# Kernel tuning notes

Measured on AMD Instinct MI355X. Metric: run time of the kernel, lower is better.

## Reference

```python
import jax, jax.numpy as jnp
import numpy as np


def setup_inputs() -> dict:
    key = jax.random.key(0)
    B, n, E, D = 128, 128, 524288, 64  # graphs, nodes/graph, original edges, edge-feat dim
    k1, k2, k3, k4 = jax.random.split(key, 4)
    g = jax.random.randint(k1, (E,), 0, B)
    src = jax.random.randint(k2, (E,), 0, n)
    dst = jax.random.randint(k3, (E,), 0, n)
    edge_index = jnp.stack([g * n + src, g * n + dst]).astype(jnp.int32)  # [2,E], within-graph edges
    edge_attr = jax.random.normal(k4, (E, D), dtype=jnp.float32)
    batch = jnp.repeat(jnp.arange(B, dtype=jnp.int32), n)  # [N] node -> graph id
    return {"edge_index": edge_index, "edge_attr": edge_attr, "batch": batch,
            "num_graphs": B, "n_per_graph": n}


def reference(edge_index, edge_attr, batch, num_graphs, n_per_graph):
    """Pad edge set to the full per-graph adjacency (incl. self-loops, as the
    torch code's ones().nonzero() does) and coalesce with op='add'.
    Equal-sized graphs => full edge list has static shape [2, B*n*n], already
    unique and row-major sorted, matching torch_sparse.coalesce output order."""
    B, n = num_graphs, n_per_graph
    D = edge_attr.shape[1]
    gid = jnp.arange(B, dtype=edge_index.dtype)[:, None, None]  # [B,1,1]
    loc = jnp.arange(n, dtype=edge_index.dtype)
    rows = jnp.broadcast_to(gid * n + loc[None, :, None], (B, n, n)).reshape(-1)
    cols = jnp.broadcast_to(gid * n + loc[None, None, :], (B, n, n)).reshape(-1)
    out_idx = jnp.stack([rows, cols])  # [2, B*n*n]
    # position of each original edge inside the full (sorted) edge list
    r, c = edge_index[0], edge_index[1]
    g = batch[r].astype(r.dtype)
    pos = g * (n * n) + (r - g * n) * n + (c - g * n)  # [E]
    # coalesce op='add': zeros for padded edges, sum original attrs on duplicates
    out_val = jnp.zeros((B * n * n, D), dtype=edge_attr.dtype).at[pos].add(edge_attr)
    return out_idx, out_val
```

## Files before the change

kernel.cpp:

```cpp
#include <hip/hip_runtime.h>


typedef float vfloat4 __attribute__((ext_vector_type(4)));

__global__ void build_chain_kernel(const int* __restrict__ ei,
                                   const int* __restrict__ batch,
                                   int* __restrict__ head,
                                   int* __restrict__ next,
                                   int E, int n, int n2) {
    int e = blockIdx.x * blockDim.x + threadIdx.x;
    if (e >= E) return;
    int r = ei[e];
    int c = ei[E + e];
    int g = batch[r];
    int pos = g * n2 + (r - g * n) * n + (c - g * n);
    next[e] = atomicExch(&head[pos], e);
}

template <int CHUNKS>
__global__ void gather_occupied_kernel(const float* __restrict__ ea,
                                       const int* __restrict__ head,
                                       const int* __restrict__ next,
                                       float* __restrict__ vals,
                                       int M, int D) {
    unsigned tid = blockIdx.x * blockDim.x + threadIdx.x;
    unsigned q, ch;
    if (CHUNKS > 0) {
        q = tid / (unsigned)CHUNKS;
        ch = tid & (unsigned)(CHUNKS - 1);
    } else {
        unsigned chunks = (unsigned)(D >> 2);
        q = tid / chunks;
        ch = tid - q * chunks;
    }
    if (q >= (unsigned)M) return;

    int e = head[q];
    if (e < 0) return;

    vfloat4 acc = {0.f, 0.f, 0.f, 0.f};
    do {
        const vfloat4 v = *(const vfloat4*)(ea + (size_t)e * D + ch * 4);
        acc += v;
        e = next[e];
    } while (e >= 0);
    __builtin_nontemporal_store(acc, (vfloat4*)(vals + (size_t)q * D + ch * 4));
}

__global__ void fill_idx_kernel(float* __restrict__ rows,
                                float* __restrict__ cols,
                                int M, int n, int n2) {
    int q0 = (blockIdx.x * blockDim.x + threadIdx.x) * 4;
    if (q0 >= M) return;
    float4 rv, cv;
    int q = q0;
    rv.x = (float)(q / n); cv.x = (float)((q / n2) * n + (q % n)); q++;
    rv.y = (float)(q / n); cv.y = (float)((q / n2) * n + (q % n)); q++;
    rv.z = (float)(q / n); cv.z = (float)((q / n2) * n + (q % n)); q++;
    rv.w = (float)(q / n); cv.w = (float)((q / n2) * n + (q % n));
    *(float4*)(rows + q0) = rv;
    *(float4*)(cols + q0) = cv;
}

__global__ void scatter_add_kernel(const int* __restrict__ ei,
                                   const float* __restrict__ ea,
                                   const int* __restrict__ batch,
                                   float* __restrict__ vals,
                                   int E, int D, int n, int n2) {
    int chunksPerEdge = D >> 2;
    long long tid = (long long)blockIdx.x * blockDim.x + threadIdx.x;
    int e = (int)(tid / chunksPerEdge);
    int ch = (int)(tid % chunksPerEdge);
    if (e >= E) return;
    int r = ei[e];
    int c = ei[E + e];
    int g = batch[r];
    long long pos = (long long)g * n2 + (long long)(r - g * n) * n + (long long)(c - g * n);
    float4 src = *(const float4*)(ea + (long long)e * D + ch * 4);
    float* dst = vals + pos * D + ch * 4;
    atomicAdd(dst + 0, src.x);
    atomicAdd(dst + 1, src.y);
    atomicAdd(dst + 2, src.z);
    atomicAdd(dst + 3, src.w);
}

extern "C" void kernel_launch(void* const* d_in, const int* in_sizes, int n_in,
                              void* d_out, int out_size, void* d_ws, size_t ws_size,
                              hipStream_t stream) {
    const int* edge_index = (const int*)d_in[0];
    const float* edge_attr = (const float*)d_in[1];
    const int* batch = (const int*)d_in[2];

    const int E  = in_sizes[0] / 2;
    const int D  = in_sizes[1] / E;
    const int M  = out_size / (D + 2);
    const int BN = in_sizes[2];
    const int n  = M / BN;
    const int n2 = n * n;

    float* rows = (float*)d_out;
    float* cols = rows + M;
    float* vals = cols + M;

    const size_t ws_need = ((size_t)M + (size_t)E) * sizeof(int);
    if (ws_size >= ws_need && (D & 3) == 0) {
        int* head = (int*)d_ws;
        int* next = head + M;

        (void)hipMemsetAsync(vals, 0, (size_t)M * D * sizeof(float), stream);
        (void)hipMemsetAsync(head, 0xFF, (size_t)M * sizeof(int), stream);

        {
            int block = 256;
            int grid = (E + block - 1) / block;
            build_chain_kernel<<<grid, block, 0, stream>>>(
                edge_index, batch, head, next, E, n, n2);
        }
        {
            long long total = (long long)M * (D / 4);
            int block = 256;
            long long grid = (total + block - 1) / block;
            if (D == 64) {
                gather_occupied_kernel<16><<<(int)grid, block, 0, stream>>>(
                    edge_attr, head, next, vals, M, D);
            } else {
                gather_occupied_kernel<0><<<(int)grid, block, 0, stream>>>(
                    edge_attr, head, next, vals, M, D);
            }
        }
        {
            int threads = (M + 3) / 4;
            int block = 256;
            int grid = (threads + block - 1) / block;
            fill_idx_kernel<<<grid, block, 0, stream>>>(rows, cols, M, n, n2);
        }
    } else {
        (void)hipMemsetAsync(vals, 0, (size_t)M * D * sizeof(float), stream);
        {
            int threads = (M + 3) / 4;
            int block = 256;
            int grid = (threads + block - 1) / block;
            fill_idx_kernel<<<grid, block, 0, stream>>>(rows, cols, M, n, n2);
        }
        {
            long long total = (long long)E * (D / 4);
            int block = 256;
            long long grid = (total + block - 1) / block;
            scatter_add_kernel<<<(int)grid, block, 0, stream>>>(
                edge_index, edge_attr, batch, vals, E, D, n, n2);
        }
    }
}
```

Before: 732.0 us.

## Fuse zero-fill into gather kernel and use grid-stride loop

Removes the separate memset of the output values and has the gather kernel write zeros for empty adjacency slots itself, so each output element is written once. The gather becomes a grid-stride loop capped at 8192 blocks, with the next-pointer load issued before the accumulate. The aim is to avoid a second full pass over the large output buffer. In exchange every slot is now visited and stored by the kernel, including empty ones, and the capped grid may give less latency hiding.

```diff
diff --git a/kernel.cpp b/kernel.cpp
--- a/kernel.cpp
+++ b/kernel.cpp
@@ -18,33 +18,34 @@
 }
 
 template <int CHUNKS>
-__global__ void gather_occupied_kernel(const float* __restrict__ ea,
-                                       const int* __restrict__ head,
-                                       const int* __restrict__ next,
-                                       float* __restrict__ vals,
-                                       int M, int D) {
-    unsigned tid = blockIdx.x * blockDim.x + threadIdx.x;
-    unsigned q, ch;
-    if (CHUNKS > 0) {
-        q = tid / (unsigned)CHUNKS;
-        ch = tid & (unsigned)(CHUNKS - 1);
-    } else {
-        unsigned chunks = (unsigned)(D >> 2);
-        q = tid / chunks;
-        ch = tid - q * chunks;
+__global__ __launch_bounds__(256) void fused_vals_kernel(
+        const float* __restrict__ ea,
+        const int* __restrict__ head,
+        const int* __restrict__ next,
+        float* __restrict__ vals,
+        long long total, int D) {
+    const long long stride = (long long)gridDim.x * blockDim.x;
+    for (long long tid = (long long)blockIdx.x * blockDim.x + threadIdx.x;
+         tid < total; tid += stride) {
+        unsigned q, ch;
+        if (CHUNKS > 0) {
+            q  = (unsigned)(tid / CHUNKS);
+            ch = (unsigned)tid & (unsigned)(CHUNKS - 1);
+        } else {
+            unsigned chunks = (unsigned)(D >> 2);
+            q  = (unsigned)(tid / chunks);
+            ch = (unsigned)(tid - (long long)q * chunks);
+        }
+        int e = head[q];
+        vfloat4 acc = {0.f, 0.f, 0.f, 0.f};
+        while (e >= 0) {
+            const vfloat4 v = *(const vfloat4*)(ea + (size_t)e * D + ch * 4);
+            int nx = next[e];
+            acc += v;
+            e = nx;
+        }
+        __builtin_nontemporal_store(acc, (vfloat4*)(vals + (size_t)q * D + ch * 4));
     }
-    if (q >= (unsigned)M) return;
-
-    int e = head[q];
-    if (e < 0) return;
-
-    vfloat4 acc = {0.f, 0.f, 0.f, 0.f};
-    do {
-        const vfloat4 v = *(const vfloat4*)(ea + (size_t)e * D + ch * 4);
-        acc += v;
-        e = next[e];
-    } while (e >= 0);
-    __builtin_nontemporal_store(acc, (vfloat4*)(vals + (size_t)q * D + ch * 4));
 }
 
 __global__ void fill_idx_kernel(float* __restrict__ rows,
@@ -107,7 +108,6 @@
         int* head = (int*)d_ws;
         int* next = head + M;
 
-        (void)hipMemsetAsync(vals, 0, (size_t)M * D * sizeof(float), stream);
         (void)hipMemsetAsync(head, 0xFF, (size_t)M * sizeof(int), stream);
 
         {
@@ -119,13 +119,15 @@
         {
             long long total = (long long)M * (D / 4);
             int block = 256;
-            long long grid = (total + block - 1) / block;
+            int grid = 8192;
+            long long blocks_needed = (total + block - 1) / block;
+            if (blocks_needed < grid) grid = (int)blocks_needed;
             if (D == 64) {
-                gather_occupied_kernel<16><<<(int)grid, block, 0, stream>>>(
-                    edge_attr, head, next, vals, M, D);
+                fused_vals_kernel<16><<<grid, block, 0, stream>>>(
+                    edge_attr, head, next, vals, total, D);
             } else {
-                gather_occupied_kernel<0><<<(int)grid, block, 0, stream>>>(
-                    edge_attr, head, next, vals, M, D);
+                fused_vals_kernel<0><<<grid, block, 0, stream>>>(
+                    edge_attr, head, next, vals, total, D);
             }
         }
         {
```

Measured after the change: 699.6 us. 4.4% less time.
